# Performance work log

Measured on AMD Instinct MI355X. Metric: run time of the kernel, lower is better.

Reference implementation:

```python
import jax, jax.numpy as jnp
import numpy as np

N = 2048            # adj_size (num nodes)
F = 512             # in_features
M = 10              # m_chebyshev (polynomial order)
Q = 64              # Chebyshev-Gauss quadrature points for coefficients
HK_THRESHOLD = 1e-5 # args.hk_threshold


def setup_inputs() -> dict:
    key = jax.random.key(0)
    k1, k2 = jax.random.split(key, 2)
    x = jax.random.normal(k1, (N, F), dtype=jnp.float32)
    # random sparse symmetric adjacency -> normalized Laplacian P_n = I - D^-1/2 A D^-1/2
    u = jax.random.uniform(k2, (N, N), dtype=jnp.float32)
    a = (u < (16.0 / N)).astype(jnp.float32)
    a = jnp.maximum(a, a.T) * (1.0 - jnp.eye(N, dtype=jnp.float32))
    dinv = 1.0 / jnp.sqrt(jnp.clip(a.sum(1), 1.0, None))
    P_n = jnp.eye(N, dtype=jnp.float32) - dinv[:, None] * a * dinv[None, :]
    t = jnp.full((N,), -2.0, dtype=jnp.float32)  # Parameter init fill_(-2.0)
    eigmax = jnp.ones((1,), dtype=jnp.float32) * 2.0  # spectral bound of normalized Laplacian
    return {"x": x, "P_n": P_n, "t": t, "eigmax": eigmax}


def _cheb_coeffs(t, eigmax):
    # Per-node Chebyshev coefficients c[i,k] of exp(-exp(t_i) * lam),
    # lam = (eigmax/2)*(xhat+1), xhat in [-1,1]; computed with Chebyshev-Gauss
    # quadrature (numerically exact DCT form of the Bessel-function coefficients).
    s = jnp.exp(t)                                   # [N] per-node diffusion scale > 0
    theta = jnp.pi * (jnp.arange(Q, dtype=jnp.float32) + 0.5) / Q   # [Q]
    lam = (eigmax * 0.5) * (jnp.cos(theta) + 1.0)    # [Q] sampled eigenvalues
    w = jnp.exp(-s[:, None] * lam[None, :])          # [N,Q] exp(-s*lam)
    ck = jnp.cos(jnp.arange(M + 1, dtype=jnp.float32)[:, None] * theta[None, :])  # [M+1,Q]
    c = (2.0 / Q) * jnp.einsum('nq,kq->nk', w, ck)   # [N,M+1]
    return c.at[:, 0].mul(0.5)


def reference(x, P_n, t, eigmax):
    eigmax = eigmax.reshape(())
    c = _cheb_coeffs(t, eigmax)                       # [N,M+1]
    eye = jnp.eye(N, dtype=P_n.dtype)
    L_hat = (2.0 / eigmax) * P_n - eye                # scaled Laplacian, spectrum in [-1,1]
    # Chebyshev recurrence T_0=I, T_1=L_hat, T_k = 2 L_hat T_{k-1} - T_{k-2}
    T_prev, T_cur = eye, L_hat
    H = c[:, 0:1] * T_prev + c[:, 1:2] * T_cur        # per-row (per-node) coefficients
    for k in range(2, M + 1):
        T_prev, T_cur = T_cur, 2.0 * (L_hat @ T_cur) - T_prev
        H = H + c[:, k:k + 1] * T_cur
    H = jnp.where(H < HK_THRESHOLD, 0.0, H)           # hk[hk < hk_threshold] = 0
    output = H @ x                                    # [N,F]
    return output, t
```

## Files before the change

### kernel.cpp

```cpp
#include <hip/hip_runtime.h>
#include <hip/hip_fp16.h>

#define NN   2048
#define NF   512
#define MCH  10
#define QQ   64
#define KMAX 128
#define TOL  2e-3f
#define PI_F 3.14159265358979323846f

__device__ inline float2 h2f2(unsigned u) { return __half22float2(*(__half2*)&u); }
__device__ inline unsigned f2h2(float a, float b) {
    __half2 h = __floats2half2_rn(a, b);
    return *(unsigned*)&h;
}

__global__ __launch_bounds__(256) void xpose_in(const float* __restrict__ x,
                                                unsigned short* __restrict__ xT,
                                                float* __restrict__ pmax) {
    __shared__ float tile[64][65];
    __shared__ float wm[4];
    int r0 = blockIdx.x * 64;
    int f0 = blockIdx.y * 64;
    int tx = threadIdx.x & 63, ty = threadIdx.x >> 6;
    float m = 0.f;
#pragma unroll
    for (int i = 0; i < 16; ++i) {
        int rr = ty * 16 + i;
        float v = x[(size_t)(r0 + rr) * NF + f0 + tx];
        tile[rr][tx] = v;
        m = fmaxf(m, fabsf(v));
    }
    __syncthreads();
#pragma unroll
    for (int i = 0; i < 16; ++i) {
        int ff = ty * 16 + i;
        __half h = __float2half_rn(tile[tx][ff]);
        xT[(size_t)(f0 + ff) * NN + r0 + tx] = __half_as_ushort(h);
    }
#pragma unroll
    for (int o = 32; o > 0; o >>= 1) m = fmaxf(m, __shfl_down(m, o));
    if ((threadIdx.x & 63) == 0) wm[threadIdx.x >> 6] = m;
    __syncthreads();
    if (threadIdx.x == 0)
        pmax[blockIdx.y * 32 + blockIdx.x] = fmaxf(fmaxf(wm[0], wm[1]), fmaxf(wm[2], wm[3]));
}

__global__ __launch_bounds__(256) void csr_coeff(const float* __restrict__ P,
                                                 const float* __restrict__ eigmax,
                                                 const float* __restrict__ t,
                                                 unsigned* __restrict__ packed,
                                                 int* __restrict__ lens,
                                                 float* __restrict__ cc_cm,
                                                 float* __restrict__ out) {
    int row = blockIdx.x;
    __shared__ int cnt;
    if (threadIdx.x == 0) cnt = 0;
    __syncthreads();
    float em = eigmax[0];
    float s2 = 2.0f / em;
    for (int j = threadIdx.x; j < NN; j += 256) {
        float v = s2 * P[(size_t)row * NN + j] - (j == row ? 1.0f : 0.0f);
        if (v != 0.0f) {
            int p = atomicAdd(&cnt, 1);
            if (p < KMAX) {
                unsigned short hb = __half_as_ushort(__float2half_rn(v));
                packed[(size_t)p * NN + row] = ((unsigned)j << 18) | (unsigned)hb;
            }
        }
    }
    if (threadIdx.x < QQ) {
        int q = threadIdx.x;
        float th = PI_F * ((float)q + 0.5f) / (float)QQ;
        float ct = cosf(th);
        float s  = expf(t[row]);
        float w  = __expf(-s * em * 0.5f * (ct + 1.0f));
        float tk[MCH + 1];
        tk[0] = w;
        tk[1] = w * ct;
        float pm = 1.f, pc = ct;
#pragma unroll
        for (int k = 2; k <= MCH; ++k) {
            float nx = 2.f * ct * pc - pm;
            tk[k] = w * nx;
            pm = pc; pc = nx;
        }
#pragma unroll
        for (int o = 32; o > 0; o >>= 1) {
#pragma unroll
            for (int k = 0; k <= MCH; ++k) tk[k] += __shfl_down(tk[k], o);
        }
        if (q == 0) {
#pragma unroll
            for (int k = 0; k <= MCH; ++k) {
                float v = tk[k] * (2.0f / (float)QQ);
                if (k == 0) v *= 0.5f;
                cc_cm[k * NN + row] = v;
            }
        }
    }
    __syncthreads();
    if (threadIdx.x == 0) {
        lens[row] = min(cnt, KMAX);
        out[(size_t)NN * NF + row] = t[row];
    }
}

__global__ __launch_bounds__(1024) void cheb_fused(
    const unsigned short* __restrict__ xT, const float* __restrict__ pmax,
    const float* __restrict__ cc_cm,
    const unsigned* __restrict__ packed, const int* __restrict__ lens,
    float* __restrict__ outT) {
    __shared__ unsigned S[2][NN];
    __shared__ float redf[16];
    __shared__ int   redi[16];

    const int tid  = threadIdx.x;
    const int lane = tid & 63;
    const int wid  = tid >> 6;
    const int c0   = blockIdx.x * 2;
    const int r0   = tid;
    const int r1   = tid + 1024;

    float cA[MCH + 1], cB[MCH + 1];
#pragma unroll
    for (int k = 0; k <= MCH; ++k) {
        cA[k] = cc_cm[k * NN + r0];
        cB[k] = cc_cm[k * NN + r1];
    }

    float B = (tid < 256) ? pmax[tid] : 0.f;
#pragma unroll
    for (int o = 32; o > 0; o >>= 1) B = fmaxf(B, __shfl_down(B, o));
    if (lane == 0) redf[wid] = B;
    __syncthreads();
    B = redf[lane & 15];
#pragma unroll
    for (int o = 8; o > 0; o >>= 1) B = fmaxf(B, __shfl_down(B, o));
    B = __shfl(B, 0);
    const float bound = 45.2548f * B;

    float tail0 = 0.f, tail1 = 0.f;
    int Ki = 1;
#pragma unroll
    for (int k = MCH; k >= 2; --k) {
        tail0 += fabsf(cA[k]);
        tail1 += fabsf(cB[k]);
        if (fmaxf(tail0, tail1) * bound > TOL) { Ki = k; break; }
    }
#pragma unroll
    for (int o = 32; o > 0; o >>= 1) Ki = max(Ki, __shfl_down(Ki, o));
    if (lane == 0) redi[wid] = Ki;
    __syncthreads();
    Ki = redi[lane & 15];
#pragma unroll
    for (int o = 8; o > 0; o >>= 1) Ki = max(Ki, __shfl_down(Ki, o));
    const int K = __shfl(Ki, 0);

    unsigned X0 = (unsigned)xT[(size_t)c0 * NN + r0] |
                  ((unsigned)xT[(size_t)(c0 + 1) * NN + r0] << 16);
    unsigned X1 = (unsigned)xT[(size_t)c0 * NN + r1] |
                  ((unsigned)xT[(size_t)(c0 + 1) * NN + r1] << 16);
    S[0][r0] = X0;
    S[0][r1] = X1;
    const int len0 = lens[r0];
    const int len1 = lens[r1];
    __syncthreads();

    auto gather = [&](int buf, int r, int len) -> unsigned {
        const char* Sb = (const char*)S[buf];
        unsigned accu = 0u;
        __half2 acc = *(__half2*)&accu;
#pragma unroll 8
        for (int e = 0; e < len; ++e) {
            unsigned pk = packed[(size_t)e * NN + r];
            unsigned g  = *(const unsigned*)(Sb + (pk >> 16));
            unsigned v2 = __builtin_amdgcn_perm(pk, pk, 0x01000100u);
            acc = __hfma2(*(__half2*)&v2, *(__half2*)&g, acc);
        }
        return *(unsigned*)&acc;
    };

    unsigned A0 = gather(0, r0, len0);
    unsigned A1 = gather(0, r1, len1);
    S[1][r0] = A0;
    S[1][r1] = A1;
    float2 xf0 = h2f2(X0), xf1 = h2f2(X1);
    float2 yf0 = h2f2(A0), yf1 = h2f2(A1);
    float2 H0 = make_float2(cA[0] * xf0.x + cA[1] * yf0.x, cA[0] * xf0.y + cA[1] * yf0.y);
    float2 H1 = make_float2(cB[0] * xf1.x + cB[1] * yf1.x, cB[0] * xf1.y + cB[1] * yf1.y);

    int cur = 1;
#pragma unroll
    for (int k = 2; k <= MCH; ++k) {
        if (k > K) break;
        __syncthreads();
        unsigned G0 = gather(cur, r0, len0);
        unsigned G1 = gather(cur, r1, len1);
        int oth = cur ^ 1;
        float2 gf0 = h2f2(G0), gf1 = h2f2(G1);
        float2 pf0 = h2f2(S[oth][r0]), pf1 = h2f2(S[oth][r1]);
        float2 t0 = make_float2(2.f * gf0.x - pf0.x, 2.f * gf0.y - pf0.y);
        float2 t1 = make_float2(2.f * gf1.x - pf1.x, 2.f * gf1.y - pf1.y);
        __syncthreads();
        S[oth][r0] = f2h2(t0.x, t0.y);
        S[oth][r1] = f2h2(t1.x, t1.y);
        H0.x += cA[k] * t0.x; H0.y += cA[k] * t0.y;
        H1.x += cB[k] * t1.x; H1.y += cB[k] * t1.y;
        cur = oth;
    }

    outT[(size_t)c0 * NN + r0]       = H0.x;
    outT[(size_t)(c0 + 1) * NN + r0] = H0.y;
    outT[(size_t)c0 * NN + r1]       = H1.x;
    outT[(size_t)(c0 + 1) * NN + r1] = H1.y;
}

__global__ __launch_bounds__(256) void xpose_out(const float* __restrict__ outT,
                                                 float* __restrict__ out) {
    __shared__ float tile[64][65];
    int f0 = blockIdx.x * 64;
    int r0 = blockIdx.y * 64;
    int tx = threadIdx.x & 63, ty = threadIdx.x >> 6;
#pragma unroll
    for (int i = 0; i < 16; ++i) {
        int ff = ty * 16 + i;
        tile[ff][tx] = outT[(size_t)(f0 + ff) * NN + r0 + tx];
    }
    __syncthreads();
#pragma unroll
    for (int i = 0; i < 16; ++i) {
        int rr = ty * 16 + i;
        out[(size_t)(r0 + rr) * NF + f0 + tx] = tile[tx][rr];
    }
}

extern "C" void kernel_launch(void* const* d_in, const int* in_sizes, int n_in,
                              void* d_out, int out_size, void* d_ws, size_t ws_size,
                              hipStream_t stream) {
    const float* x      = (const float*)d_in[0];
    const float* P_n    = (const float*)d_in[1];
    const float* t      = (const float*)d_in[2];
    const float* eigmax = (const float*)d_in[3];
    float* out = (float*)d_out;

    char* p = (char*)d_ws;
    auto carve = [&](size_t bytes) -> void* {
        void* r = (void*)p;
        p += (bytes + 255) & ~(size_t)255;
        return r;
    };
    unsigned*       packed = (unsigned*)      carve((size_t)KMAX * NN * sizeof(unsigned));
    int*            lens   = (int*)           carve((size_t)NN * sizeof(int));
    float*          cc_cm  = (float*)         carve((size_t)(MCH + 1) * NN * sizeof(float));
    float*          pmax   = (float*)         carve((size_t)256 * sizeof(float));
    unsigned short* xT     = (unsigned short*)carve((size_t)NF * NN * sizeof(unsigned short));
    float*          outT   = (float*)         carve((size_t)NF * NN * sizeof(float));

    xpose_in<<<dim3(NN / 64, NF / 64), dim3(256), 0, stream>>>(x, xT, pmax);
    csr_coeff<<<dim3(NN), dim3(256), 0, stream>>>(P_n, eigmax, t, packed, lens, cc_cm, out);
    cheb_fused<<<dim3(NF / 2), dim3(1024), 0, stream>>>(xT, pmax, cc_cm, packed, lens, outT);
    xpose_out<<<dim3(NF / 64, NN / 64), dim3(256), 0, stream>>>(outT, out);
}
```

Before: 107.6 us.

## Merge prep kernels and process four feature columns per Chebyshev block

Merges the x transpose and CSR/coefficient kernels into one launch, which removes one kernel launch. The Chebyshev kernel now handles four feature columns per block using 8-byte LDS entries, so each sparse index/value load is reused across four columns. That halves the block count to 128, fewer than the GPU's compute units, and doubles LDS per block. Coefficients are now read from global memory inside the loop instead of being held in registers. The packed column index shift changes from 18 to 19 so that the byte offset matches the 8-byte LDS stride.

```diff
diff --git a/kernel.cpp b/kernel.cpp
--- a/kernel.cpp
+++ b/kernel.cpp
@@ -15,94 +15,96 @@
     return *(unsigned*)&h;
 }
 
-__global__ __launch_bounds__(256) void xpose_in(const float* __restrict__ x,
-                                                unsigned short* __restrict__ xT,
-                                                float* __restrict__ pmax) {
-    __shared__ float tile[64][65];
-    __shared__ float wm[4];
-    int r0 = blockIdx.x * 64;
-    int f0 = blockIdx.y * 64;
-    int tx = threadIdx.x & 63, ty = threadIdx.x >> 6;
-    float m = 0.f;
-#pragma unroll
-    for (int i = 0; i < 16; ++i) {
-        int rr = ty * 16 + i;
-        float v = x[(size_t)(r0 + rr) * NF + f0 + tx];
-        tile[rr][tx] = v;
-        m = fmaxf(m, fabsf(v));
-    }
-    __syncthreads();
-#pragma unroll
-    for (int i = 0; i < 16; ++i) {
-        int ff = ty * 16 + i;
-        __half h = __float2half_rn(tile[tx][ff]);
-        xT[(size_t)(f0 + ff) * NN + r0 + tx] = __half_as_ushort(h);
-    }
-#pragma unroll
-    for (int o = 32; o > 0; o >>= 1) m = fmaxf(m, __shfl_down(m, o));
-    if ((threadIdx.x & 63) == 0) wm[threadIdx.x >> 6] = m;
-    __syncthreads();
-    if (threadIdx.x == 0)
-        pmax[blockIdx.y * 32 + blockIdx.x] = fmaxf(fmaxf(wm[0], wm[1]), fmaxf(wm[2], wm[3]));
-}
-
-__global__ __launch_bounds__(256) void csr_coeff(const float* __restrict__ P,
-                                                 const float* __restrict__ eigmax,
-                                                 const float* __restrict__ t,
-                                                 unsigned* __restrict__ packed,
-                                                 int* __restrict__ lens,
-                                                 float* __restrict__ cc_cm,
-                                                 float* __restrict__ out) {
-    int row = blockIdx.x;
-    __shared__ int cnt;
-    if (threadIdx.x == 0) cnt = 0;
-    __syncthreads();
-    float em = eigmax[0];
-    float s2 = 2.0f / em;
-    for (int j = threadIdx.x; j < NN; j += 256) {
-        float v = s2 * P[(size_t)row * NN + j] - (j == row ? 1.0f : 0.0f);
-        if (v != 0.0f) {
-            int p = atomicAdd(&cnt, 1);
-            if (p < KMAX) {
-                unsigned short hb = __half_as_ushort(__float2half_rn(v));
-                packed[(size_t)p * NN + row] = ((unsigned)j << 18) | (unsigned)hb;
-            }
-        }
-    }
-    if (threadIdx.x < QQ) {
-        int q = threadIdx.x;
-        float th = PI_F * ((float)q + 0.5f) / (float)QQ;
-        float ct = cosf(th);
-        float s  = expf(t[row]);
-        float w  = __expf(-s * em * 0.5f * (ct + 1.0f));
-        float tk[MCH + 1];
-        tk[0] = w;
-        tk[1] = w * ct;
-        float pm = 1.f, pc = ct;
-#pragma unroll
-        for (int k = 2; k <= MCH; ++k) {
-            float nx = 2.f * ct * pc - pm;
-            tk[k] = w * nx;
-            pm = pc; pc = nx;
-        }
-#pragma unroll
-        for (int o = 32; o > 0; o >>= 1) {
-#pragma unroll
-            for (int k = 0; k <= MCH; ++k) tk[k] += __shfl_down(tk[k], o);
-        }
-        if (q == 0) {
-#pragma unroll
-            for (int k = 0; k <= MCH; ++k) {
-                float v = tk[k] * (2.0f / (float)QQ);
-                if (k == 0) v *= 0.5f;
-                cc_cm[k * NN + row] = v;
-            }
-        }
-    }
-    __syncthreads();
-    if (threadIdx.x == 0) {
-        lens[row] = min(cnt, KMAX);
-        out[(size_t)NN * NF + row] = t[row];
+__global__ __launch_bounds__(256) void prep(const float* __restrict__ P,
+                                            const float* __restrict__ eigmax,
+                                            const float* __restrict__ t,
+                                            const float* __restrict__ x,
+                                            unsigned* __restrict__ packed,
+                                            int* __restrict__ lens,
+                                            float* __restrict__ cc_cm,
+                                            float* __restrict__ pmax,
+                                            unsigned short* __restrict__ xT,
+                                            float* __restrict__ out) {
+    int bid = blockIdx.x;
+    if (bid < 256) {
+        __shared__ float tile[64][65];
+        __shared__ float wm[4];
+        int r0 = (bid & 31) * 64;
+        int f0 = (bid >> 5) * 64;
+        int tx = threadIdx.x & 63, ty = threadIdx.x >> 6;
+        float m = 0.f;
+#pragma unroll
+        for (int i = 0; i < 16; ++i) {
+            int rr = ty * 16 + i;
+            float v = x[(size_t)(r0 + rr) * NF + f0 + tx];
+            tile[rr][tx] = v;
+            m = fmaxf(m, fabsf(v));
+        }
+        __syncthreads();
+#pragma unroll
+        for (int i = 0; i < 16; ++i) {
+            int ff = ty * 16 + i;
+            __half h = __float2half_rn(tile[tx][ff]);
+            xT[(size_t)(f0 + ff) * NN + r0 + tx] = __half_as_ushort(h);
+        }
+#pragma unroll
+        for (int o = 32; o > 0; o >>= 1) m = fmaxf(m, __shfl_down(m, o));
+        if ((threadIdx.x & 63) == 0) wm[threadIdx.x >> 6] = m;
+        __syncthreads();
+        if (threadIdx.x == 0)
+            pmax[bid] = fmaxf(fmaxf(wm[0], wm[1]), fmaxf(wm[2], wm[3]));
+    } else {
+        int row = bid - 256;
+        __shared__ int cnt;
+        if (threadIdx.x == 0) cnt = 0;
+        __syncthreads();
+        float em = eigmax[0];
+        float s2 = 2.0f / em;
+        for (int j = threadIdx.x; j < NN; j += 256) {
+            float v = s2 * P[(size_t)row * NN + j] - (j == row ? 1.0f : 0.0f);
+            if (v != 0.0f) {
+                int p = atomicAdd(&cnt, 1);
+                if (p < KMAX) {
+                    unsigned short hb = __half_as_ushort(__float2half_rn(v));
+                    packed[(size_t)p * NN + row] = ((unsigned)j << 19) | (unsigned)hb;
+                }
+            }
+        }
+        if (threadIdx.x < QQ) {
+            int q = threadIdx.x;
+            float th = PI_F * ((float)q + 0.5f) / (float)QQ;
+            float ct = cosf(th);
+            float s  = expf(t[row]);
+            float w  = __expf(-s * em * 0.5f * (ct + 1.0f));
+            float tk[MCH + 1];
+            tk[0] = w;
+            tk[1] = w * ct;
+            float pm = 1.f, pc = ct;
+#pragma unroll
+            for (int k = 2; k <= MCH; ++k) {
+                float nx = 2.f * ct * pc - pm;
+                tk[k] = w * nx;
+                pm = pc; pc = nx;
+            }
+#pragma unroll
+            for (int o = 32; o > 0; o >>= 1) {
+#pragma unroll
+                for (int k = 0; k <= MCH; ++k) tk[k] += __shfl_down(tk[k], o);
+            }
+            if (q == 0) {
+#pragma unroll
+                for (int k = 0; k <= MCH; ++k) {
+                    float v = tk[k] * (2.0f / (float)QQ);
+                    if (k == 0) v *= 0.5f;
+                    cc_cm[k * NN + row] = v;
+                }
+            }
+        }
+        __syncthreads();
+        if (threadIdx.x == 0) {
+            lens[row] = min(cnt, KMAX);
+            out[(size_t)NN * NF + row] = t[row];
+        }
     }
 }
 
@@ -111,23 +113,16 @@
     const float* __restrict__ cc_cm,
     const unsigned* __restrict__ packed, const int* __restrict__ lens,
     float* __restrict__ outT) {
-    __shared__ unsigned S[2][NN];
+    __shared__ uint2 S[2][NN];
     __shared__ float redf[16];
     __shared__ int   redi[16];
 
     const int tid  = threadIdx.x;
     const int lane = tid & 63;
     const int wid  = tid >> 6;
-    const int c0   = blockIdx.x * 2;
+    const int c0   = blockIdx.x * 4;
     const int r0   = tid;
     const int r1   = tid + 1024;
-
-    float cA[MCH + 1], cB[MCH + 1];
-#pragma unroll
-    for (int k = 0; k <= MCH; ++k) {
-        cA[k] = cc_cm[k * NN + r0];
-        cB[k] = cc_cm[k * NN + r1];
-    }
 
     float B = (tid < 256) ? pmax[tid] : 0.f;
 #pragma unroll
@@ -142,10 +137,9 @@
 
     float tail0 = 0.f, tail1 = 0.f;
     int Ki = 1;
-#pragma unroll
     for (int k = MCH; k >= 2; --k) {
-        tail0 += fabsf(cA[k]);
-        tail1 += fabsf(cB[k]);
+        tail0 += fabsf(cc_cm[k * NN + r0]);
+        tail1 += fabsf(cc_cm[k * NN + r1]);
         if (fmaxf(tail0, tail1) * bound > TOL) { Ki = k; break; }
     }
 #pragma unroll
@@ -157,63 +151,92 @@
     for (int o = 8; o > 0; o >>= 1) Ki = max(Ki, __shfl_down(Ki, o));
     const int K = __shfl(Ki, 0);
 
-    unsigned X0 = (unsigned)xT[(size_t)c0 * NN + r0] |
-                  ((unsigned)xT[(size_t)(c0 + 1) * NN + r0] << 16);
-    unsigned X1 = (unsigned)xT[(size_t)c0 * NN + r1] |
-                  ((unsigned)xT[(size_t)(c0 + 1) * NN + r1] << 16);
+    uint2 X0, X1;
+    X0.x = (unsigned)xT[(size_t)(c0 + 0) * NN + r0] |
+           ((unsigned)xT[(size_t)(c0 + 1) * NN + r0] << 16);
+    X0.y = (unsigned)xT[(size_t)(c0 + 2) * NN + r0] |
+           ((unsigned)xT[(size_t)(c0 + 3) * NN + r0] << 16);
+    X1.x = (unsigned)xT[(size_t)(c0 + 0) * NN + r1] |
+           ((unsigned)xT[(size_t)(c0 + 1) * NN + r1] << 16);
+    X1.y = (unsigned)xT[(size_t)(c0 + 2) * NN + r1] |
+           ((unsigned)xT[(size_t)(c0 + 3) * NN + r1] << 16);
     S[0][r0] = X0;
     S[0][r1] = X1;
     const int len0 = lens[r0];
     const int len1 = lens[r1];
     __syncthreads();
 
-    auto gather = [&](int buf, int r, int len) -> unsigned {
+    auto gather = [&](int buf, int r, int len) -> uint2 {
         const char* Sb = (const char*)S[buf];
-        unsigned accu = 0u;
-        __half2 acc = *(__half2*)&accu;
+        unsigned z = 0u;
+        __half2 a01 = *(__half2*)&z, a23 = *(__half2*)&z;
 #pragma unroll 8
         for (int e = 0; e < len; ++e) {
             unsigned pk = packed[(size_t)e * NN + r];
-            unsigned g  = *(const unsigned*)(Sb + (pk >> 16));
+            uint2 g = *(const uint2*)(Sb + (pk >> 16));
             unsigned v2 = __builtin_amdgcn_perm(pk, pk, 0x01000100u);
-            acc = __hfma2(*(__half2*)&v2, *(__half2*)&g, acc);
-        }
-        return *(unsigned*)&acc;
+            a01 = __hfma2(*(__half2*)&v2, *(__half2*)&g.x, a01);
+            a23 = __hfma2(*(__half2*)&v2, *(__half2*)&g.y, a23);
+        }
+        uint2 ret;
+        ret.x = *(unsigned*)&a01;
+        ret.y = *(unsigned*)&a23;
+        return ret;
     };
 
-    unsigned A0 = gather(0, r0, len0);
-    unsigned A1 = gather(0, r1, len1);
+    uint2 A0 = gather(0, r0, len0);
+    uint2 A1 = gather(0, r1, len1);
     S[1][r0] = A0;
     S[1][r1] = A1;
-    float2 xf0 = h2f2(X0), xf1 = h2f2(X1);
-    float2 yf0 = h2f2(A0), yf1 = h2f2(A1);
-    float2 H0 = make_float2(cA[0] * xf0.x + cA[1] * yf0.x, cA[0] * xf0.y + cA[1] * yf0.y);
-    float2 H1 = make_float2(cB[0] * xf1.x + cB[1] * yf1.x, cB[0] * xf1.y + cB[1] * yf1.y);
+    float cA0 = cc_cm[r0], cA1 = cc_cm[NN + r0];
+    float cB0 = cc_cm[r1], cB1 = cc_cm[NN + r1];
+    float2 x01_0 = h2f2(X0.x), x23_0 = h2f2(X0.y);
+    float2 x01_1 = h2f2(X1.x), x23_1 = h2f2(X1.y);
+    float2 y01_0 = h2f2(A0.x), y23_0 = h2f2(A0.y);
+    float2 y01_1 = h2f2(A1.x), y23_1 = h2f2(A1.y);
+    float2 H01_0 = make_float2(cA0 * x01_0.x + cA1 * y01_0.x, cA0 * x01_0.y + cA1 * y01_0.y);
+    float2 H23_0 = make_float2(cA0 * x23_0.x + cA1 * y23_0.x, cA0 * x23_0.y + cA1 * y23_0.y);
+    float2 H01_1 = make_float2(cB0 * x01_1.x + cB1 * y01_1.x, cB0 * x01_1.y + cB1 * y01_1.y);
+    float2 H23_1 = make_float2(cB0 * x23_1.x + cB1 * y23_1.x, cB0 * x23_1.y + cB1 * y23_1.y);
 
     int cur = 1;
-#pragma unroll
-    for (int k = 2; k <= MCH; ++k) {
-        if (k > K) break;
-        __syncthreads();
-        unsigned G0 = gather(cur, r0, len0);
-        unsigned G1 = gather(cur, r1, len1);
+    for (int k = 2; k <= K; ++k) {
+        __syncthreads();
+        uint2 G0 = gather(cur, r0, len0);
+        uint2 G1 = gather(cur, r1, len1);
         int oth = cur ^ 1;
-        float2 gf0 = h2f2(G0), gf1 = h2f2(G1);
-        float2 pf0 = h2f2(S[oth][r0]), pf1 = h2f2(S[oth][r1]);
-        float2 t0 = make_float2(2.f * gf0.x - pf0.x, 2.f * gf0.y - pf0.y);
-        float2 t1 = make_float2(2.f * gf1.x - pf1.x, 2.f * gf1.y - pf1.y);
-        __syncthreads();
-        S[oth][r0] = f2h2(t0.x, t0.y);
-        S[oth][r1] = f2h2(t1.x, t1.y);
-        H0.x += cA[k] * t0.x; H0.y += cA[k] * t0.y;
-        H1.x += cB[k] * t1.x; H1.y += cB[k] * t1.y;
+        uint2 P0 = S[oth][r0], P1 = S[oth][r1];
+        float2 g01_0 = h2f2(G0.x), g23_0 = h2f2(G0.y);
+        float2 g01_1 = h2f2(G1.x), g23_1 = h2f2(G1.y);
+        float2 p01_0 = h2f2(P0.x), p23_0 = h2f2(P0.y);
+        float2 p01_1 = h2f2(P1.x), p23_1 = h2f2(P1.y);
+        float2 t01_0 = make_float2(2.f * g01_0.x - p01_0.x, 2.f * g01_0.y - p01_0.y);
+        float2 t23_0 = make_float2(2.f * g23_0.x - p23_0.x, 2.f * g23_0.y - p23_0.y);
+        float2 t01_1 = make_float2(2.f * g01_1.x - p01_1.x, 2.f * g01_1.y - p01_1.y);
+        float2 t23_1 = make_float2(2.f * g23_1.x - p23_1.x, 2.f * g23_1.y - p23_1.y);
+        __syncthreads();
+        uint2 T0, T1;
+        T0.x = f2h2(t01_0.x, t01_0.y);  T0.y = f2h2(t23_0.x, t23_0.y);
+        T1.x = f2h2(t01_1.x, t01_1.y);  T1.y = f2h2(t23_1.x, t23_1.y);
+        S[oth][r0] = T0;
+        S[oth][r1] = T1;
+        float ckA = cc_cm[k * NN + r0];
+        float ckB = cc_cm[k * NN + r1];
+        H01_0.x += ckA * t01_0.x; H01_0.y += ckA * t01_0.y;
+        H23_0.x += ckA * t23_0.x; H23_0.y += ckA * t23_0.y;
+        H01_1.x += ckB * t01_1.x; H01_1.y += ckB * t01_1.y;
+        H23_1.x += ckB * t23_1.x; H23_1.y += ckB * t23_1.y;
         cur = oth;
     }
 
-    outT[(size_t)c0 * NN + r0]       = H0.x;
-    outT[(size_t)(c0 + 1) * NN + r0] = H0.y;
-    outT[(size_t)c0 * NN + r1]       = H1.x;
-    outT[(size_t)(c0 + 1) * NN + r1] = H1.y;
+    outT[(size_t)(c0 + 0) * NN + r0] = H01_0.x;
+    outT[(size_t)(c0 + 1) * NN + r0] = H01_0.y;
+    outT[(size_t)(c0 + 2) * NN + r0] = H23_0.x;
+    outT[(size_t)(c0 + 3) * NN + r0] = H23_0.y;
+    outT[(size_t)(c0 + 0) * NN + r1] = H01_1.x;
+    outT[(size_t)(c0 + 1) * NN + r1] = H01_1.y;
+    outT[(size_t)(c0 + 2) * NN + r1] = H23_1.x;
+    outT[(size_t)(c0 + 3) * NN + r1] = H23_1.y;
 }
 
 __global__ __launch_bounds__(256) void xpose_out(const float* __restrict__ outT,
@@ -257,8 +280,9 @@
     unsigned short* xT     = (unsigned short*)carve((size_t)NF * NN * sizeof(unsigned short));
     float*          outT   = (float*)         carve((size_t)NF * NN * sizeof(float));
 
-    xpose_in<<<dim3(NN / 64, NF / 64), dim3(256), 0, stream>>>(x, xT, pmax);
-    csr_coeff<<<dim3(NN), dim3(256), 0, stream>>>(P_n, eigmax, t, packed, lens, cc_cm, out);
-    cheb_fused<<<dim3(NF / 2), dim3(1024), 0, stream>>>(xT, pmax, cc_cm, packed, lens, outT);
+    prep<<<dim3(256 + NN), dim3(256), 0, stream>>>(P_n, eigmax, t, x, packed, lens,
+                                                   cc_cm, pmax, xT, out);
+    cheb_fused<<<dim3(NF / 4), dim3(1024), 0, stream>>>(xT, pmax, cc_cm,
+                                                        packed, lens, outT);
     xpose_out<<<dim3(NF / 64, NN / 64), dim3(256), 0, stream>>>(outT, out);
 }
```

New measurement: 111.6 us. +3.8%, slower.
